# Kernel optimization log

Measured on AMD Instinct MI355X. Metric: run time of the kernel, lower is better.

Reference implementation:

```python
import jax, jax.numpy as jnp
import numpy as np

K = 7          # median window size
PAD = (K - 1) // 2  # same padding with stride 1


def setup_inputs() -> dict:
    key = jax.random.key(0)
    x = jax.random.uniform(key, (8, 3, 512, 512), dtype=jnp.float32)
    return {"x": x}


def _median_pool_hardtanh(x):
    B, C, H, W = x.shape
    # reflect pad, same as F.pad(..., mode='reflect') with (pl,pr,pt,pb)=(3,3,3,3)
    xp = jnp.pad(x, ((0, 0), (0, 0), (PAD, PAD), (PAD, PAD)), mode='reflect')
    # Gather the 49 shifted views of the padded image (fixed small loop over
    # kernel offsets, vectorized over B,C,H,W). Shape: [B,C,H,W,49]
    patches = jnp.stack(
        [xp[:, :, i:i + H, j:j + W] for i in range(K) for j in range(K)],
        axis=-1,
    )
    # torch .median(dim=-1) over an odd count (49) equals the true median
    med = jnp.median(patches, axis=-1)
    # Hardtanh(min_val=0, max_val=1)
    return jnp.clip(med, 0.0, 1.0)


def reference(x):
    return _median_pool_hardtanh(x)
```

## Files before the change

kernel.cpp:

```cpp
#include <hip/hip_runtime.h>

#define DEV __device__ __forceinline__

template <int N> struct V { float v[N == 0 ? 1 : N]; };

template <int M, int N>
DEV V<M + N> mrg(V<M> a, V<N> b) {
    V<M + N> o;
    if constexpr (M == 0) {
#pragma unroll
        for (int i = 0; i < N; ++i) o.v[i] = b.v[i];
    } else if constexpr (N == 0) {
#pragma unroll
        for (int i = 0; i < M; ++i) o.v[i] = a.v[i];
    } else if constexpr (M == 1 && N == 1) {
        o.v[0] = fminf(a.v[0], b.v[0]);
        o.v[1] = fmaxf(a.v[0], b.v[0]);
    } else if constexpr ((M & 1) && (N & 1)) {
        constexpr int AE = (M + 1) / 2, AO = M / 2, BE = (N + 1) / 2, BO = N / 2;
        V<AE> ae; V<AO> ao; V<BE> be; V<BO> bo;
#pragma unroll
        for (int i = 0; i < AE; ++i) ae.v[i] = a.v[2 * i];
#pragma unroll
        for (int i = 0; i < AO; ++i) ao.v[i] = a.v[2 * i + 1];
#pragma unroll
        for (int i = 0; i < BE; ++i) be.v[i] = b.v[2 * i];
#pragma unroll
        for (int i = 0; i < BO; ++i) bo.v[i] = b.v[2 * i + 1];
        V<AE + BO> E = mrg<AE, BO>(ae, bo);
        V<AO + BE> O = mrg<AO, BE>(ao, be);
        constexpr int P = AE + BO;
#pragma unroll
        for (int i = 0; i < P; ++i) {
            o.v[2 * i] = fminf(E.v[i], O.v[i]);
            o.v[2 * i + 1] = fmaxf(E.v[i], O.v[i]);
        }
    } else {
        constexpr int AE = (M + 1) / 2, AO = M / 2, BE = (N + 1) / 2, BO = N / 2;
        V<AE> ae; V<AO> ao; V<BE> be; V<BO> bo;
#pragma unroll
        for (int i = 0; i < AE; ++i) ae.v[i] = a.v[2 * i];
#pragma unroll
        for (int i = 0; i < AO; ++i) ao.v[i] = a.v[2 * i + 1];
#pragma unroll
        for (int i = 0; i < BE; ++i) be.v[i] = b.v[2 * i];
#pragma unroll
        for (int i = 0; i < BO; ++i) bo.v[i] = b.v[2 * i + 1];
        V<AE + BE> E = mrg<AE, BE>(ae, be);
        V<AO + BO> O = mrg<AO, BO>(ao, bo);
        constexpr int CEn = AE + BE, COn = AO + BO;
        o.v[0] = E.v[0];
#pragma unroll
        for (int i = 0; i < COn; ++i) {
            if (i + 1 < CEn) {
                o.v[2 * i + 1] = fminf(O.v[i], E.v[i + 1]);
                o.v[2 * i + 2] = fmaxf(O.v[i], E.v[i + 1]);
            } else {
                o.v[2 * i + 1] = O.v[i];
            }
        }
    }
    return o;
}

DEV void ce(float& a, float& b) {
    float lo = fminf(a, b);
    b = fmaxf(a, b);
    a = lo;
}

DEV V<7> sort7(V<7> x) {
    ce(x.v[1], x.v[2]); ce(x.v[0], x.v[2]); ce(x.v[0], x.v[1]);
    ce(x.v[3], x.v[4]); ce(x.v[5], x.v[6]); ce(x.v[3], x.v[5]);
    ce(x.v[4], x.v[6]); ce(x.v[4], x.v[5]);
    V<3> a; a.v[0] = x.v[0]; a.v[1] = x.v[1]; a.v[2] = x.v[2];
    V<4> b; b.v[0] = x.v[3]; b.v[1] = x.v[4]; b.v[2] = x.v[5]; b.v[3] = x.v[6];
    return mrg<3, 4>(a, b);
}

DEV float sel24(V<28> Q, V<21> F) {
    float m = Q.v[24];
#pragma unroll
    for (int i = 4; i < 25; ++i) m = fminf(m, fmaxf(Q.v[i - 1], F.v[24 - i]));
    return m;
}

static constexpr int W = 512, H = 512, PLANE = W * H;

__global__ __launch_bounds__(256, 1) void median7_hardtanh_kernel(
    const float* __restrict__ in, float* __restrict__ out) {
    int local = (int)threadIdx.x;
    int tx = local & 127;
    int ry = local >> 7;
    int r = blockIdx.x * 2 + ry;
    int y = r & (H - 1);
    int p = r >> 9;
    const float* img = in + (size_t)p * PLANE;
    int x0 = tx * 4;

    int rows[7];
#pragma unroll
    for (int i = 0; i < 7; ++i) {
        int t = y + i - 3;
        t = (t < 0) ? -t : t;
        t = (t > H - 1) ? 2 * (H - 1) - t : t;
        rows[i] = t << 9;
    }

    V<7> c0, c1, c2, c3, c4, c5, c6, c7, c8, c9;
    if (x0 >= 4 && x0 <= W - 8) {
#pragma unroll
        for (int i = 0; i < 7; ++i) {
            const float* rp = img + rows[i] + x0;
            float4 L = *reinterpret_cast<const float4*>(rp - 4);
            float4 C = *reinterpret_cast<const float4*>(rp);
            float4 R = *reinterpret_cast<const float4*>(rp + 4);
            c0.v[i] = L.y; c1.v[i] = L.z; c2.v[i] = L.w;
            c3.v[i] = C.x; c4.v[i] = C.y; c5.v[i] = C.z; c6.v[i] = C.w;
            c7.v[i] = R.x; c8.v[i] = R.y; c9.v[i] = R.z;
        }
    } else {
        int cols[10];
#pragma unroll
        for (int j = 0; j < 10; ++j) {
            int u = x0 + j - 3;
            u = (u < 0) ? -u : u;
            u = (u > W - 1) ? 2 * (W - 1) - u : u;
            cols[j] = u;
        }
#pragma unroll
        for (int i = 0; i < 7; ++i) {
            const float* rp = img + rows[i];
            c0.v[i] = rp[cols[0]]; c1.v[i] = rp[cols[1]]; c2.v[i] = rp[cols[2]];
            c3.v[i] = rp[cols[3]]; c4.v[i] = rp[cols[4]]; c5.v[i] = rp[cols[5]];
            c6.v[i] = rp[cols[6]]; c7.v[i] = rp[cols[7]]; c8.v[i] = rp[cols[8]];
            c9.v[i] = rp[cols[9]];
        }
    }

    c0 = sort7(c0); c1 = sort7(c1); c2 = sort7(c2); c3 = sort7(c3);
    c4 = sort7(c4); c5 = sort7(c5); c6 = sort7(c6); c7 = sort7(c7);
    c8 = sort7(c8); c9 = sort7(c9);

    V<28> Q = mrg<14, 14>(mrg<7, 7>(c3, c4), mrg<7, 7>(c5, c6));
    V<14> P12 = mrg<7, 7>(c1, c2);
    V<14> P78 = mrg<7, 7>(c7, c8);

    float m0 = sel24(Q, mrg<14, 7>(P12, c0));
    float m1 = sel24(Q, mrg<14, 7>(P12, c7));
    float m2 = sel24(Q, mrg<14, 7>(P78, c2));
    float m3 = sel24(Q, mrg<14, 7>(P78, c9));

    float4 o;
    o.x = fminf(fmaxf(m0, 0.0f), 1.0f);
    o.y = fminf(fmaxf(m1, 0.0f), 1.0f);
    o.z = fminf(fmaxf(m2, 0.0f), 1.0f);
    o.w = fminf(fmaxf(m3, 0.0f), 1.0f);
    *reinterpret_cast<float4*>(out + (size_t)r * W + x0) = o;
}

extern "C" void kernel_launch(void* const* d_in, const int* in_sizes, int n_in,
                              void* d_out, int out_size, void* d_ws, size_t ws_size,
                              hipStream_t stream) {
    const float* x = (const float*)d_in[0];
    float* outp = (float*)d_out;
    int rows_total = out_size / W;
    int blocks = rows_total / 2;
    median7_hardtanh_kernel<<<blocks, 256, 0, stream>>>(x, outp);
}
```

Baseline: 132.3 us.

## Use fmed3 sort3, tree-reduce selection, swizzle blocks, relax occupancy bound

Replaces the 3-element sorting network in sort7 with min/max/fmed3 instructions and turns the serial fminf chain in sel24 into a balanced tree reduction, shortening the dependency chain. Blocks are remapped with an XCD-style swizzle (bid&7)*768 so that consecutive rows land on the same chiplet for L2 locality. The launch bound now allows up to 2 waves per EU instead of forcing 1, which trades register headroom for occupancy. The swizzle hardcodes 6144 blocks, so it only fits this input size.

```diff
diff --git a/kernel.cpp b/kernel.cpp
--- a/kernel.cpp
+++ b/kernel.cpp
@@ -70,29 +70,44 @@
 }
 
 DEV V<7> sort7(V<7> x) {
-    ce(x.v[1], x.v[2]); ce(x.v[0], x.v[2]); ce(x.v[0], x.v[1]);
-    ce(x.v[3], x.v[4]); ce(x.v[5], x.v[6]); ce(x.v[3], x.v[5]);
-    ce(x.v[4], x.v[6]); ce(x.v[4], x.v[5]);
-    V<3> a; a.v[0] = x.v[0]; a.v[1] = x.v[1]; a.v[2] = x.v[2];
-    V<4> b; b.v[0] = x.v[3]; b.v[1] = x.v[4]; b.v[2] = x.v[5]; b.v[3] = x.v[6];
-    return mrg<3, 4>(a, b);
+    float a = x.v[0], b = x.v[1], c = x.v[2];
+    V<3> s3;
+    s3.v[0] = fminf(fminf(a, b), c);
+    s3.v[1] = __builtin_amdgcn_fmed3f(a, b, c);
+    s3.v[2] = fmaxf(fmaxf(a, b), c);
+    ce(x.v[3], x.v[4]); ce(x.v[5], x.v[6]);
+    ce(x.v[3], x.v[5]); ce(x.v[4], x.v[6]); ce(x.v[4], x.v[5]);
+    V<4> s4;
+    s4.v[0] = x.v[3]; s4.v[1] = x.v[4]; s4.v[2] = x.v[5]; s4.v[3] = x.v[6];
+    return mrg<3, 4>(s3, s4);
 }
 
-DEV float sel24(V<28> Q, V<21> F) {
-    float m = Q.v[24];
+DEV float sel24(const V<28>& Q, const V<21>& F) {
+    float t[22];
+    t[21] = Q.v[24];
 #pragma unroll
-    for (int i = 4; i < 25; ++i) m = fminf(m, fmaxf(Q.v[i - 1], F.v[24 - i]));
-    return m;
+    for (int i = 4; i < 25; ++i) t[i - 4] = fmaxf(Q.v[i - 1], F.v[24 - i]);
+#pragma unroll
+    for (int i = 0; i < 11; ++i) t[i] = fminf(t[i], t[i + 11]);
+#pragma unroll
+    for (int i = 0; i < 5; ++i) t[i] = fminf(t[i], t[i + 6]);
+#pragma unroll
+    for (int i = 0; i < 3; ++i) t[i] = fminf(t[i], t[i + 3]);
+    return fminf(fminf(t[0], t[1]), t[2]);
 }
 
 static constexpr int W = 512, H = 512, PLANE = W * H;
 
-__global__ __launch_bounds__(256, 1) void median7_hardtanh_kernel(
-    const float* __restrict__ in, float* __restrict__ out) {
+__global__ __launch_bounds__(256) __attribute__((amdgpu_waves_per_eu(1, 2)))
+void median7_hardtanh_kernel(const float* __restrict__ in,
+                             float* __restrict__ out) {
+    int bid = (int)blockIdx.x;
+    int swz = (bid & 7) * 768 + (bid >> 3);
+
     int local = (int)threadIdx.x;
     int tx = local & 127;
     int ry = local >> 7;
-    int r = blockIdx.x * 2 + ry;
+    int r = swz * 2 + ry;
     int y = r & (H - 1);
     int p = r >> 9;
     const float* img = in + (size_t)p * PLANE;
```

Measured after the change: 148.6 us. 12.3% more time.
